# Kernel tuning notes

Measured on AMD Instinct MI355X. Metric: run time of the kernel, lower is better.

## Reference

```python
import jax, jax.numpy as jnp
import numpy as np

B, S, N, D, M = 4, 4096, 16, 64, 4  # batch, seq, heads, head_dim, num_scales

def setup_inputs() -> dict:
    key = jax.random.key(0)
    ks = jax.random.split(key, 6)
    return {
        "q": jax.random.normal(ks[0], (B, S, N, D), dtype=jnp.float32),
        "k": jax.random.normal(ks[1], (B, S, N, D), dtype=jnp.float32),
        "v": jax.random.normal(ks[2], (B, S, N, D), dtype=jnp.float32),
        "memory": jax.random.normal(ks[3], (B, M, N, D, D), dtype=jnp.float32),
        "decay_factors": jax.random.uniform(ks[4], (M,), dtype=jnp.float32) + 0.5,
        "gate_weights": jax.random.uniform(ks[5], (M,), dtype=jnp.float32),
    }

def reference(q, k, v, memory, decay_factors, gate_weights):
    # --- update_memory: decayed outer-product accumulation ---
    # new_info[b,n,k,v] = sum_s k[b,s,n,k] * v[b,s,n,v]  (fused; never build [b,s,n,k,v])
    new_info = jnp.einsum('bsnk,bsnv->bnkv', k, v)
    sig = jax.nn.sigmoid(decay_factors)            # [M]
    sig5 = sig[None, :, None, None, None]          # [1,M,1,1,1]
    mem_new = memory * sig5 + (1.0 - sig5) * new_info[:, None]  # [B,M,N,D,D]
    # --- forward read: q @ memory per scale, softmax-gated scale mixing ---
    gates = jax.nn.softmax(gate_weights)           # [M]
    # fuse gate mixing into the contraction; never build [b,m,s,n,v]
    out = jnp.einsum('bsnk,bmnkv,m->bsnv', q, mem_new, gates)
    return out
```

## Files before the change

### kernel.cpp

```cpp
#include <hip/hip_runtime.h>
#include <hip/hip_bf16.h>
#include <math.h>

constexpr int B = 4, S = 4096, N = 16, D = 64, M = 4;
constexpr int SND = S * N * D;
constexpr int ND  = N * D;
constexpr int DD  = D * D;
constexpr int NCH = 32;
constexpr int SPB = S / NCH;

typedef __attribute__((ext_vector_type(8))) short bf16x8;
typedef __attribute__((ext_vector_type(4))) float f32x4;
typedef unsigned short u16;
typedef unsigned int u32;

__device__ inline u16 f2bf(float x) {
  __hip_bfloat16 h = __float2bfloat16(x);
  return __builtin_bit_cast(u16, h);
}

__global__ __launch_bounds__(256) void k1_partials(const float* __restrict__ kg,
                                                   const float* __restrict__ vg,
                                                   u16* __restrict__ part) {
  __shared__ u16 kT[64][128];
  __shared__ u16 vT[64][128];

  const int t = threadIdx.x, w = t >> 6, l = t & 63;
  const int lr = l & 15, lg = l >> 4;
  const int rp = t >> 4;
  const int c  = t & 15;
  const int bn = blockIdx.x, ch = blockIdx.y;
  const int b = bn >> 4, n = bn & 15;

  const size_t base = (size_t)b * SND + (size_t)n * D + (size_t)ch * SPB * ND;

  float4 kr[8], vr[8];
#pragma unroll
  for (int st = 0; st < 4; ++st) {
    const float* kp = kg + base + (size_t)(st * 32 + 2 * rp) * ND + 4 * c;
    const float* vp = vg + base + (size_t)(st * 32 + 2 * rp) * ND + 4 * c;
    kr[2 * st]     = *(const float4*)kp;
    kr[2 * st + 1] = *(const float4*)(kp + ND);
    vr[2 * st]     = *(const float4*)vp;
    vr[2 * st + 1] = *(const float4*)(vp + ND);
  }

#pragma unroll
  for (int st = 0; st < 4; ++st) {
    const int s  = st * 32 + 2 * rp;
    const int so = s >> 3, sl = s & 7;
    const float* k0 = (const float*)&kr[2 * st];
    const float* k1 = (const float*)&kr[2 * st + 1];
    const float* v0 = (const float*)&vr[2 * st];
    const float* v1 = (const float*)&vr[2 * st + 1];
#pragma unroll
    for (int o = 0; o < 4; ++o) {
      const int d = 4 * c + o;
      const int slot = ((so ^ (d & 15)) << 3) + sl;
      *(u32*)&kT[d][slot] = (u32)f2bf(k0[o]) | ((u32)f2bf(k1[o]) << 16);
      *(u32*)&vT[d][slot] = (u32)f2bf(v0[o]) | ((u32)f2bf(v1[o]) << 16);
    }
  }

  __syncthreads();

  f32x4 acc[4];
#pragma unroll
  for (int i = 0; i < 4; ++i) acc[i] = (f32x4)0.f;

#pragma unroll
  for (int kk = 0; kk < 4; ++kk) {
    const int so = 4 * kk + lg;
    const int da = 16 * w + lr;
    bf16x8 af = *(const bf16x8*)&kT[da][(so ^ (da & 15)) << 3];
    bf16x8 bq[4];
#pragma unroll
    for (int ni = 0; ni < 4; ++ni) {
      const int db = 16 * ni + lr;
      bq[ni] = *(const bf16x8*)&vT[db][(so ^ (db & 15)) << 3];
    }
#pragma unroll
    for (int ni = 0; ni < 4; ++ni)
      acc[ni] = __builtin_amdgcn_mfma_f32_16x16x32_bf16(af, bq[ni],
                                                        acc[ni], 0, 0, 0);
  }

  u16* p = part + ((size_t)bn * NCH + ch) * DD;
#pragma unroll
  for (int ni = 0; ni < 4; ++ni)
#pragma unroll
    for (int ri = 0; ri < 4; ++ri)
      p[(16 * w + 4 * lg + ri) * 64 + 16 * ni + lr] = f2bf(acc[ni][ri]);
}

__global__ __launch_bounds__(256) void k2_combine(const u16* __restrict__ part,
                                                  const float* __restrict__ memg,
                                                  const float* __restrict__ decay,
                                                  const float* __restrict__ gatew,
                                                  u16* __restrict__ meffT) {
  const int t = threadIdx.x;
  const int bn = blockIdx.x;
  const int b = bn >> 4, n = bn & 15;
  const int kv = blockIdx.y * 256 + t;
  const int k = kv >> 6, v = kv & 63;

  float gw[M], df[M];
#pragma unroll
  for (int m = 0; m < M; ++m) { gw[m] = gatew[m]; df[m] = decay[m]; }
  const float mx = fmaxf(fmaxf(gw[0], gw[1]), fmaxf(gw[2], gw[3]));
  float e[M], esum = 0.f;
#pragma unroll
  for (int m = 0; m < M; ++m) { e[m] = expf(gw[m] - mx); esum += e[m]; }
  float wgt[M], cc = 0.f;
#pragma unroll
  for (int m = 0; m < M; ++m) {
    const float g = e[m] / esum;
    const float sg = 1.f / (1.f + expf(-df[m]));
    wgt[m] = g * sg;
    cc += g * (1.f - sg);
  }

  const u16* pb = part + (size_t)bn * NCH * DD + kv;
  float ni = 0.f;
#pragma unroll 8
  for (int ch = 0; ch < NCH; ++ch) {
    __hip_bfloat16 h = __builtin_bit_cast(__hip_bfloat16, pb[(size_t)ch * DD]);
    ni += __bfloat162float(h);
  }
  float a = cc * ni;
#pragma unroll
  for (int m = 0; m < M; ++m)
    a += wgt[m] * memg[(((size_t)b * M + m) * N + n) * DD + kv];

  meffT[(size_t)bn * DD + v * 64 + k] = f2bf(a);
}

__global__ __launch_bounds__(256, 4) void k3_out(const float* __restrict__ qg,
                                                 const u16* __restrict__ meffT,
                                                 float* __restrict__ outg) {
  const int t = threadIdx.x, w = t >> 6, l = t & 63;
  const int lr = l & 15, lg = l >> 4;
  const int bn = blockIdx.x;
  const int b = bn >> 4, n = bn & 15;
  const int s0 = blockIdx.y * 256 + w * 64;

  const u16* mb = meffT + (size_t)bn * DD;
  bf16x8 bfr[4][2];
#pragma unroll
  for (int ni = 0; ni < 4; ++ni)
#pragma unroll
    for (int ks = 0; ks < 2; ++ks)
      bfr[ni][ks] = *(const bf16x8*)(mb + (16 * ni + lr) * 64 + 32 * ks + 8 * lg);

  f32x4 acc[4][4];
#pragma unroll
  for (int i = 0; i < 4; ++i)
#pragma unroll
    for (int j = 0; j < 4; ++j) acc[i][j] = (f32x4)0.f;

  const size_t qbase = (size_t)b * SND + (size_t)n * D;

#pragma unroll
  for (int mi = 0; mi < 4; ++mi) {
    const float* qr = qg + qbase + (size_t)(s0 + 16 * mi + lr) * ND + 8 * lg;
#pragma unroll
    for (int ks = 0; ks < 2; ++ks) {
      float qa[8];
      *(float4*)&qa[0] = *(const float4*)(qr + 32 * ks);
      *(float4*)&qa[4] = *(const float4*)(qr + 32 * ks + 4);
      bf16x8 a;
#pragma unroll
      for (int j = 0; j < 8; ++j) a[j] = (short)f2bf(qa[j]);
#pragma unroll
      for (int ni = 0; ni < 4; ++ni)
        acc[mi][ni] = __builtin_amdgcn_mfma_f32_16x16x32_bf16(a, bfr[ni][ks],
                                                              acc[mi][ni], 0, 0, 0);
    }
  }

#pragma unroll
  for (int mi = 0; mi < 4; ++mi)
#pragma unroll
    for (int ni = 0; ni < 4; ++ni)
#pragma unroll
      for (int ri = 0; ri < 4; ++ri)
        outg[qbase + (size_t)(s0 + 16 * mi + 4 * lg + ri) * ND + 16 * ni + lr] =
            acc[mi][ni][ri];
}

extern "C" void kernel_launch(void* const* d_in, const int* in_sizes, int n_in,
                              void* d_out, int out_size, void* d_ws, size_t ws_size,
                              hipStream_t stream) {
  const float* q     = (const float*)d_in[0];
  const float* k     = (const float*)d_in[1];
  const float* v     = (const float*)d_in[2];
  const float* memg  = (const float*)d_in[3];
  const float* decay = (const float*)d_in[4];
  const float* gatew = (const float*)d_in[5];
  float* out = (float*)d_out;

  u16* meffT = (u16*)d_ws;
  const size_t meffT_bytes = (size_t)64 * DD * sizeof(u16);
  u16* part = (u16*)((char*)d_ws + meffT_bytes);

  hipLaunchKernelGGL(k1_partials, dim3(64, NCH), dim3(256), 0, stream,
                     k, v, part);
  hipLaunchKernelGGL(k2_combine, dim3(64, 16), dim3(256), 0, stream,
                     part, memg, decay, gatew, meffT);
  hipLaunchKernelGGL(k3_out, dim3(64, 16), dim3(256), 0, stream,
                     q, meffT, out);
}
```

Measured before the change: 66.42 us.

## Load k/v fragments directly from global into MFMA registers, halve chunk count

The partial outer-product kernel drops its LDS transpose staging and barrier. Each lane now loads its k and v scalars straight from global memory into MFMA operand registers and converts them in place. Each block now covers 256 sequence rows instead of 128, halving the number of partials that the combine kernel has to reduce. The cost is that global loads become scalar, lane-strided 4-byte accesses instead of float4, which may hurt coalescing. The second k1 CTA dimension also halves, reducing parallelism.

```diff
diff --git a/kernel.cpp b/kernel.cpp
--- a/kernel.cpp
+++ b/kernel.cpp
@@ -6,7 +6,7 @@
 constexpr int SND = S * N * D;
 constexpr int ND  = N * D;
 constexpr int DD  = D * D;
-constexpr int NCH = 32;
+constexpr int NCH = 16;
 constexpr int SPB = S / NCH;
 
 typedef __attribute__((ext_vector_type(8))) short bf16x8;
@@ -22,63 +22,38 @@
 __global__ __launch_bounds__(256) void k1_partials(const float* __restrict__ kg,
                                                    const float* __restrict__ vg,
                                                    u16* __restrict__ part) {
-  __shared__ u16 kT[64][128];
-  __shared__ u16 vT[64][128];
-
   const int t = threadIdx.x, w = t >> 6, l = t & 63;
   const int lr = l & 15, lg = l >> 4;
-  const int rp = t >> 4;
-  const int c  = t & 15;
   const int bn = blockIdx.x, ch = blockIdx.y;
   const int b = bn >> 4, n = bn & 15;
 
   const size_t base = (size_t)b * SND + (size_t)n * D + (size_t)ch * SPB * ND;
-
-  float4 kr[8], vr[8];
-#pragma unroll
-  for (int st = 0; st < 4; ++st) {
-    const float* kp = kg + base + (size_t)(st * 32 + 2 * rp) * ND + 4 * c;
-    const float* vp = vg + base + (size_t)(st * 32 + 2 * rp) * ND + 4 * c;
-    kr[2 * st]     = *(const float4*)kp;
-    kr[2 * st + 1] = *(const float4*)(kp + ND);
-    vr[2 * st]     = *(const float4*)vp;
-    vr[2 * st + 1] = *(const float4*)(vp + ND);
-  }
-
-#pragma unroll
-  for (int st = 0; st < 4; ++st) {
-    const int s  = st * 32 + 2 * rp;
-    const int so = s >> 3, sl = s & 7;
-    const float* k0 = (const float*)&kr[2 * st];
-    const float* k1 = (const float*)&kr[2 * st + 1];
-    const float* v0 = (const float*)&vr[2 * st];
-    const float* v1 = (const float*)&vr[2 * st + 1];
-#pragma unroll
-    for (int o = 0; o < 4; ++o) {
-      const int d = 4 * c + o;
-      const int slot = ((so ^ (d & 15)) << 3) + sl;
-      *(u32*)&kT[d][slot] = (u32)f2bf(k0[o]) | ((u32)f2bf(k1[o]) << 16);
-      *(u32*)&vT[d][slot] = (u32)f2bf(v0[o]) | ((u32)f2bf(v1[o]) << 16);
-    }
-  }
-
-  __syncthreads();
+  const float* kp = kg + base + 16 * w + lr;
+  const float* vp = vg + base + lr;
 
   f32x4 acc[4];
 #pragma unroll
   for (int i = 0; i < 4; ++i) acc[i] = (f32x4)0.f;
 
 #pragma unroll
-  for (int kk = 0; kk < 4; ++kk) {
-    const int so = 4 * kk + lg;
-    const int da = 16 * w + lr;
-    bf16x8 af = *(const bf16x8*)&kT[da][(so ^ (da & 15)) << 3];
-    bf16x8 bq[4];
+  for (int st = 0; st < 8; ++st) {
+    float kd[8], vd[8][4];
 #pragma unroll
-    for (int ni = 0; ni < 4; ++ni) {
-      const int db = 16 * ni + lr;
-      bq[ni] = *(const bf16x8*)&vT[db][(so ^ (db & 15)) << 3];
+    for (int j = 0; j < 8; ++j) {
+      const size_t ro = ((size_t)st * 32 + 8 * lg + j) * ND;
+      kd[j]    = kp[ro];
+      vd[j][0] = vp[ro];
+      vd[j][1] = vp[ro + 16];
+      vd[j][2] = vp[ro + 32];
+      vd[j][3] = vp[ro + 48];
     }
+    bf16x8 af, bq[4];
+#pragma unroll
+    for (int j = 0; j < 8; ++j) af[j] = (short)f2bf(kd[j]);
+#pragma unroll
+    for (int ni = 0; ni < 4; ++ni)
+#pragma unroll
+      for (int j = 0; j < 8; ++j) bq[ni][j] = (short)f2bf(vd[j][ni]);
 #pragma unroll
     for (int ni = 0; ni < 4; ++ni)
       acc[ni] = __builtin_amdgcn_mfma_f32_16x16x32_bf16(af, bq[ni],
```

New measurement: 66.59 us. About the same (+0.3%).
